# Performance work log

Hardware: AMD Instinct MI355X
Metric: run time of the kernel (lower is better)

Reference implementation:

```python
import jax, jax.numpy as jnp
import numpy as np

B, S, H, E, C, V = 512, 256, 768, 6, 10, 3


def setup_inputs() -> dict:
    key = jax.random.key(0)
    ks = jax.random.split(key, 16)

    def w(k, shape):
        fan_in = shape[-1]
        return jax.random.normal(k, shape, dtype=jnp.float32) / np.sqrt(fan_in)

    return {
        'x': jax.random.randint(ks[0], (B, S), 0, V, dtype=jnp.int64),
        'emb': w(ks[1], (V, E)),
        'W_fx': w(ks[2], (H, E)), 'W_fh': w(ks[3], (H, H)), 'b_f': w(ks[4], (H, 1)),
        'W_ix': w(ks[5], (H, E)), 'W_ih': w(ks[6], (H, H)), 'b_i': w(ks[7], (H, 1)),
        'W_ox': w(ks[8], (H, E)), 'W_oh': w(ks[9], (H, H)), 'b_o': w(ks[10], (H, 1)),
        'W_cx': w(ks[11], (H, E)), 'b_c': w(ks[12], (H, 1)),
        'W_ph': w(ks[13], (C, H)), 'b_p': w(ks[14], (C, 1)),
        'c_init': jax.random.normal(ks[15], (H, B), dtype=jnp.float32) / np.sqrt(B),
    }


def reference(x, emb, W_fx, W_fh, b_f, W_ix, W_ih, b_i, W_ox, W_oh, b_o,
              W_cx, b_c, W_ph, b_p, c_init):
    # Embed tokens: [B, S] -> [B, S, E] -> time-major [S, E, B]
    xe = jnp.transpose(emb[x], (1, 2, 0))
    xs = xe[: S - 1]  # loop runs seq_length - 1 steps

    def step(carry, x_t):
        c_prev, _ = carry  # c_prev: [H, B], x_t: [E, B]
        f_t = jax.nn.sigmoid(W_fx @ x_t + W_fh @ c_prev + b_f)
        i_t = jax.nn.sigmoid(W_ix @ x_t + W_ih @ c_prev + b_i)
        o_t = jax.nn.sigmoid(W_ox @ x_t + W_oh @ c_prev + b_o)
        c_t = jax.nn.sigmoid(W_cx @ x_t + b_c) * i_t + c_prev * f_t
        h_t = jnp.tanh(c_t) * o_t
        return (c_t, h_t), None

    h0 = jnp.zeros((H, B), dtype=c_init.dtype)
    (c_fin, h_fin), _ = jax.lax.scan(step, (c_init, h0), xs)
    p_t = W_ph @ h_fin + b_p  # [C, B]
    return jax.nn.log_softmax(p_t.T, axis=-1)  # [B, C]
```

## Files before the change

kernel.cpp:

```cpp
#include <hip/hip_runtime.h>


typedef _Float16 f16x8 __attribute__((ext_vector_type(8)));
typedef _Float16 f16x4 __attribute__((ext_vector_type(4)));
typedef float    f32x4 __attribute__((ext_vector_type(4)));

#define Hdim  768
#define Bdim  512
#define Sdim  256
#define NSTEP 255
#define Edim  6
#define NCls  10
#define NGRP  16
#define NRB   12
#define GC    32
#define HB    64
#define NKK   24
#define CSTR  776
#define XSTR  260
#define PLANE (Bdim * Hdim)
#define SCL      4096.0f
#define SCL_INV  2.44140625e-4f

#define WP_FRAGS   (2 * NRB * 4 * NKK * 64)
#define WS_CBUF    0u
#define WS_HFIN    (2u * 2u * PLANE * 2u)
#define WS_BAR     (WS_HFIN + Bdim * Hdim * 4u)
#define WS_WPK     (WS_BAR + 4096u)
#define WS_BAR_BYTES (NGRP * 16u * 4u)

__device__ __forceinline__ float sigf(float z) { return 1.0f / (1.0f + __expf(-z)); }

__device__ __forceinline__ f32x4 mf(f16x8 a, f16x8 b, f32x4 c) {
    return __builtin_amdgcn_mfma_f32_16x16x32_f16(a, b, c, 0, 0, 0);
}

__device__ __forceinline__ void keepalive(f16x8& x) {
    asm volatile("" : "+v"(x));
}

__global__ void __launch_bounds__(256)
prep_w(const float* __restrict__ Wfh, const float* __restrict__ Wih,
       _Float16* __restrict__ wpk)
{
    const int fid  = blockIdx.x * 256 + threadIdx.x;
    const int lane = fid & 63;
    const int t1   = fid >> 6;
    const int kk   = t1 % NKK;
    const int gi   = t1 / NKK;
    const int sub  = gi & 3;
    const int t3   = gi >> 2;
    const int rb   = t3 % NRB;
    const int gate = t3 / NRB;
    const int q = lane >> 4, r = lane & 15;
    const int row = rb * 64 + sub * 16 + r;
    const int col = kk * 32 + q * 8;
    const float* src = (gate ? Wih : Wfh) + (size_t)row * Hdim + col;
    f16x8 hi, lo;
    #pragma unroll
    for (int j = 0; j < 8; ++j) {
        const float v = src[j];
        const _Float16 h = (_Float16)v;
        hi[j] = h;
        lo[j] = (_Float16)((v - (float)h) * SCL);
    }
    *(f16x8*)&wpk[(size_t)fid * 8] = hi;
    *(f16x8*)&wpk[((size_t)WP_FRAGS + fid) * 8] = lo;
}

__global__ void __launch_bounds__(512, 2)
lstm_persist(const int* __restrict__ xk, const float* __restrict__ emb,
             const float* __restrict__ Wfx, const float* __restrict__ bfv,
             const float* __restrict__ Wix, const float* __restrict__ biv,
             const float* __restrict__ Wox, const float* __restrict__ Woh,
             const float* __restrict__ bov,
             const float* __restrict__ Wcx, const float* __restrict__ bcv,
             const float* __restrict__ cinit,
             const _Float16* __restrict__ wpk,
             _Float16* __restrict__ cbuf, float* __restrict__ hfin,
             unsigned int* __restrict__ bar)
{
    __shared__ __align__(16) _Float16 ldsH[GC * CSTR];
    __shared__ __align__(16) _Float16 ldsM[GC * CSTR];
    __shared__ __align__(16) float    tbl[3 * HB * 4];
    __shared__ __align__(16) float    zbuf[HB * GC];
    __shared__ __align__(4)  unsigned char xtok[GC * XSTR];
    __shared__ int s_flag;

    const int tid  = threadIdx.x;
    const int w    = tid >> 6;
    const int lane = tid & 63;
    const int q    = lane >> 4;
    const int r    = lane & 15;
    const int gt   = w >> 2;
    const int sub  = w & 3;
    const int bid  = blockIdx.x;
    const int g    = bid & 15;
    const int rb   = bid >> 4;
    const int blkh0 = rb * HB;
    const int gc0   = g * GC;
    const int hq0   = blkh0 + sub * 16 + q * 4;
    const int gi    = (gt * NRB + rb) * 4 + sub;

    if (tid == 0) s_flag = 0;
    __syncthreads();
    if (tid < 256) {
        if (xk[(size_t)gc0 * Sdim + 2 * tid + 1] != 0) s_flag = 1;
    }
    if (tid < 3 * HB) {
        const int v  = tid >> 6;
        const int hl = tid & 63;
        const int hg = blkh0 + hl;
        float pf = bfv[hg], pi = biv[hg], po = bov[hg], pc = bcv[hg];
        #pragma unroll
        for (int e = 0; e < Edim; ++e) {
            const float ev = emb[v * Edim + e];
            pf += Wfx[hg * Edim + e] * ev;
            pi += Wix[hg * Edim + e] * ev;
            po += Wox[hg * Edim + e] * ev;
            pc += Wcx[hg * Edim + e] * ev;
        }
        float* t = &tbl[(v * HB + hl) * 4];
        t[0] = pf; t[1] = pi; t[2] = po; t[3] = sigf(pc);
    }
    __syncthreads();
    const int is64 = (s_flag == 0);

    {
        const int col   = tid >> 4;
        const int sbase = (tid & 15) * 16;
        const size_t rowb = (size_t)(gc0 + col) * Sdim;
        for (int k2 = 0; k2 < 16; ++k2) {
            const int s0 = sbase + k2;
            const size_t idx = rowb + s0;
            xtok[col * XSTR + s0] = (unsigned char)xk[is64 ? (idx << 1) : idx];
        }
    }

    f16x8 whi[NKK], wlo[NKK];
    #pragma unroll
    for (int kk = 0; kk < NKK; ++kk) {
        whi[kk] = *(const f16x8*)&wpk[((size_t)(gi * NKK + kk) * 64 + lane) * 8];
        wlo[kk] = *(const f16x8*)&wpk[((size_t)WP_FRAGS + (size_t)(gi * NKK + kk) * 64 + lane) * 8];
    }
    #pragma unroll
    for (int kk = 0; kk < NKK; ++kk) {
        keepalive(whi[kk]);
        keepalive(wlo[kk]);
    }

    float cst[2][4];
    #pragma unroll
    for (int ct = 0; ct < 2; ++ct) {
        const int b = gc0 + ct * 16 + r;
        #pragma unroll
        for (int reg = 0; reg < 4; ++reg)
            cst[ct][reg] = cinit[(size_t)(hq0 + reg) * Bdim + b];
    }

    for (int i = 0; i < 48; ++i) {
        const int idx = tid + i * 512;
        const int col = idx & 31, k = idx >> 5;
        const float v = cinit[(size_t)k * Bdim + gc0 + col];
        const _Float16 h = (_Float16)v;
        ldsH[col * CSTR + k] = h;
        ldsM[col * CSTR + k] = (_Float16)((v - (float)h) * SCL);
    }

    for (int s = 0; s < NSTEP; ++s) {
        __syncthreads();

        f32x4 a0h = {0,0,0,0}, a0x = {0,0,0,0}, a1h = {0,0,0,0}, a1x = {0,0,0,0};
        #pragma unroll
        for (int kk = 0; kk < NKK; ++kk) {
            const int lo = kk * 32 + q * 8;
            const f16x8 bh0 = *(const f16x8*)&ldsH[ r       * CSTR + lo];
            const f16x8 bm0 = *(const f16x8*)&ldsM[ r       * CSTR + lo];
            const f16x8 bh1 = *(const f16x8*)&ldsH[(16 + r) * CSTR + lo];
            const f16x8 bm1 = *(const f16x8*)&ldsM[(16 + r) * CSTR + lo];
            a0h = mf(whi[kk], bh0, a0h);
            a0x = mf(whi[kk], bm0, a0x);
            a0x = mf(wlo[kk], bh0, a0x);
            a1h = mf(whi[kk], bh1, a1h);
            a1x = mf(whi[kk], bm1, a1x);
            a1x = mf(wlo[kk], bh1, a1x);
        }
        if (gt) {
            #pragma unroll
            for (int ct = 0; ct < 2; ++ct) {
                const f32x4 zh = ct ? a1h : a0h;
                const f32x4 zx = ct ? a1x : a0x;
                #pragma unroll
                for (int reg = 0; reg < 4; ++reg)
                    zbuf[(sub * 16 + q * 4 + reg) * GC + ct * 16 + r] =
                        zh[reg] + zx[reg] * SCL_INV;
            }
        }
        __syncthreads();

        if (!gt) {
            if (s != NSTEP - 1) {
                _Float16* cwH = cbuf + (size_t)(((s + 1) & 1) * 2) * PLANE;
                _Float16* cwM = cwH + PLANE;
                #pragma unroll
                for (int ct = 0; ct < 2; ++ct) {
                    const int bl = ct * 16 + r;
                    const int v  = xtok[bl * XSTR + s];
                    const float* tb = &tbl[(v * HB + sub * 16 + q * 4) * 4];
                    const f32x4 zh = ct ? a1h : a0h;
                    const f32x4 zx = ct ? a1x : a0x;
                    f16x4 cvh, cvm;
                    #pragma unroll
                    for (int reg = 0; reg < 4; ++reg) {
                        const float zf = zh[reg] + zx[reg] * SCL_INV;
                        const float zi = zbuf[(sub * 16 + q * 4 + reg) * GC + bl];
                        const float* tt = tb + reg * 4;
                        const float fg = sigf(zf + tt[0]);
                        const float ig = sigf(zi + tt[1]);
                        const float cn = tt[3] * ig + cst[ct][reg] * fg;
                        cst[ct][reg] = cn;
                        const _Float16 ch = (_Float16)cn;
                        cvh[reg] = ch;
                        cvm[reg] = (_Float16)((cn - (float)ch) * SCL);
                    }
                    unsigned long long uh, um;
                    __builtin_memcpy(&uh, &cvh, 8);
                    __builtin_memcpy(&um, &cvm, 8);
                    const size_t eo = (size_t)(gc0 + bl) * Hdim + hq0;
                    __hip_atomic_store((unsigned long long*)&cwH[eo], uh,
                                       __ATOMIC_RELAXED, __HIP_MEMORY_SCOPE_AGENT);
                    __hip_atomic_store((unsigned long long*)&cwM[eo], um,
                                       __ATOMIC_RELAXED, __HIP_MEMORY_SCOPE_AGENT);
                }
            } else {
                f32x4 o0h = {0,0,0,0}, o0x = {0,0,0,0}, o1h = {0,0,0,0}, o1x = {0,0,0,0};
                const int arow = blkh0 + sub * 16 + r;
                #pragma unroll
                for (int kk = 0; kk < NKK; ++kk) {
                    const float* wp = Woh + (size_t)arow * Hdim + kk * 32 + q * 8;
                    f16x8 who;
                    #pragma unroll
                    for (int j = 0; j < 8; ++j) who[j] = (_Float16)wp[j];
                    const int lo = kk * 32 + q * 8;
                    const f16x8 bh0 = *(const f16x8*)&ldsH[ r       * CSTR + lo];
                    const f16x8 bm0 = *(const f16x8*)&ldsM[ r       * CSTR + lo];
                    const f16x8 bh1 = *(const f16x8*)&ldsH[(16 + r) * CSTR + lo];
                    const f16x8 bm1 = *(const f16x8*)&ldsM[(16 + r) * CSTR + lo];
                    o0h = mf(who, bh0, o0h);  o0x = mf(who, bm0, o0x);
                    o1h = mf(who, bh1, o1h);  o1x = mf(who, bm1, o1x);
                }
                #pragma unroll
                for (int ct = 0; ct < 2; ++ct) {
                    const int bl = ct * 16 + r;
                    const int v  = xtok[bl * XSTR + s];
                    const float* tb = &tbl[(v * HB + sub * 16 + q * 4) * 4];
                    const f32x4 zh = ct ? a1h : a0h;
                    const f32x4 zx = ct ? a1x : a0x;
                    const f32x4 zoh = ct ? o1h : o0h;
                    const f32x4 zox = ct ? o1x : o0x;
                    f32x4 hv;
                    #pragma unroll
                    for (int reg = 0; reg < 4; ++reg) {
                        const float zf = zh[reg] + zx[reg] * SCL_INV;
                        const float zi = zbuf[(sub * 16 + q * 4 + reg) * GC + bl];
                        const float zo = zoh[reg] + zox[reg] * SCL_INV;
                        const float* tt = tb + reg * 4;
                        const float fg = sigf(zf + tt[0]);
                        const float ig = sigf(zi + tt[1]);
                        const float og = sigf(zo + tt[2]);
                        const float cn = tt[3] * ig + cst[ct][reg] * fg;
                        const float e  = __expf(-2.0f * fabsf(cn));
                        const float th = __builtin_copysignf((1.0f - e) / (1.0f + e), cn);
                        hv[reg] = th * og;
                    }
                    *(f32x4*)&hfin[(size_t)(gc0 + bl) * Hdim + hq0] = hv;
                }
            }
        }

        if (s < NSTEP - 1) {
            asm volatile("s_waitcnt vmcnt(0)" ::: "memory");
            __syncthreads();
            if (w == 0) {
                if (lane == 0)
                    __hip_atomic_store(&bar[g * 16 + rb], (unsigned)(s + 1),
                                       __ATOMIC_RELAXED, __HIP_MEMORY_SCOPE_AGENT);
                const unsigned tgt = (unsigned)(s + 1);
                while (true) {
                    unsigned vv = tgt;
                    if (lane < NRB)
                        vv = __hip_atomic_load(&bar[g * 16 + lane],
                                               __ATOMIC_RELAXED, __HIP_MEMORY_SCOPE_AGENT);
                    if (__all(vv >= tgt)) break;
                    __builtin_amdgcn_s_sleep(2);
                }
            }
            __syncthreads();
            const _Float16* crH = cbuf + (size_t)(((s + 1) & 1) * 2) * PLANE;
            const _Float16* crM = crH + PLANE;
            const int col = tid >> 4, j = tid & 15;
            const size_t rowo = (size_t)(gc0 + col) * Hdim;
            {
                unsigned long long th[12];
                #pragma unroll
                for (int i = 0; i < 12; ++i)
                    th[i] = __hip_atomic_load((unsigned long long*)&crH[rowo + (j + 16 * i) * 4],
                                              __ATOMIC_RELAXED, __HIP_MEMORY_SCOPE_AGENT);
                #pragma unroll
                for (int i = 0; i < 12; ++i)
                    *(unsigned long long*)&ldsH[col * CSTR + (j + 16 * i) * 4] = th[i];
            }
            {
                unsigned long long tm[12];
                #pragma unroll
                for (int i = 0; i < 12; ++i)
                    tm[i] = __hip_atomic_load((unsigned long long*)&crM[rowo + (j + 16 * i) * 4],
                                              __ATOMIC_RELAXED, __HIP_MEMORY_SCOPE_AGENT);
                #pragma unroll
                for (int i = 0; i < 12; ++i)
                    *(unsigned long long*)&ldsM[col * CSTR + (j + 16 * i) * 4] = tm[i];
            }
        }
    }
}

__global__ void __launch_bounds__(64)
proj_kernel(const float* __restrict__ hfin, const float* __restrict__ Wph,
            const float* __restrict__ bpv, float* __restrict__ out)
{
    const int b = blockIdx.x;
    const int lane = threadIdx.x;
    float acc[NCls];
    #pragma unroll
    for (int c = 0; c < NCls; ++c) acc[c] = 0.f;
    const float* hb = &hfin[(size_t)b * Hdim];
    for (int i = 0; i < Hdim / 64; ++i) {
        const float hv = hb[lane + i * 64];
        #pragma unroll
        for (int c = 0; c < NCls; ++c)
            acc[c] += Wph[c * Hdim + lane + i * 64] * hv;
    }
    #pragma unroll
    for (int c = 0; c < NCls; ++c) {
        float v = acc[c];
        #pragma unroll
        for (int off = 32; off > 0; off >>= 1)
            v += __shfl_xor(v, off, 64);
        acc[c] = v + bpv[c];
    }
    float m = acc[0];
    #pragma unroll
    for (int c = 1; c < NCls; ++c) m = fmaxf(m, acc[c]);
    float ssum = 0.f;
    #pragma unroll
    for (int c = 0; c < NCls; ++c) ssum += __expf(acc[c] - m);
    const float lse = m + __logf(ssum);
    if (lane < NCls) out[b * NCls + lane] = acc[lane] - lse;
}

extern "C" void kernel_launch(void* const* d_in, const int* in_sizes, int n_in,
                              void* d_out, int out_size, void* d_ws, size_t ws_size,
                              hipStream_t stream)
{
    const int*   xk    = (const int*)d_in[0];
    const float* emb   = (const float*)d_in[1];
    const float* Wfx   = (const float*)d_in[2];
    const float* Wfh   = (const float*)d_in[3];
    const float* bfv   = (const float*)d_in[4];
    const float* Wix   = (const float*)d_in[5];
    const float* Wih   = (const float*)d_in[6];
    const float* biv   = (const float*)d_in[7];
    const float* Wox   = (const float*)d_in[8];
    const float* Woh   = (const float*)d_in[9];
    const float* bov   = (const float*)d_in[10];
    const float* Wcx   = (const float*)d_in[11];
    const float* bcv   = (const float*)d_in[12];
    const float* Wph   = (const float*)d_in[13];
    const float* bpv   = (const float*)d_in[14];
    const float* cinit = (const float*)d_in[15];

    char* ws = (char*)d_ws;
    _Float16*     cbuf = (_Float16*)(ws + WS_CBUF);
    float*        hfin = (float*)(ws + WS_HFIN);
    unsigned int* bar  = (unsigned int*)(ws + WS_BAR);
    _Float16*     wpk  = (_Float16*)(ws + WS_WPK);

    hipMemsetAsync(bar, 0, WS_BAR_BYTES, stream);

    prep_w<<<dim3(WP_FRAGS / 256), dim3(256), 0, stream>>>(Wfh, Wih, wpk);

    lstm_persist<<<dim3(NGRP * NRB), dim3(512), 0, stream>>>(
        xk, emb, Wfx, bfv, Wix, biv, Wox, Woh, bov, Wcx, bcv,
        cinit, wpk, cbuf, hfin, bar);

    proj_kernel<<<dim3(Bdim), dim3(64), 0, stream>>>(hfin, Wph, bpv, (float*)d_out);
}
```

Baseline: 2.119 ms.

## Split K dimension across wave pairs with LDS reduction in LSTM step

Each wave now computes two 16-row subtiles over half of the K range instead of one subtile over the full K. Partial sums are exchanged through LDS: forget-gate partials go through a pairwise swap buffer, and input-gate partials go through two padded planes. The aim is to give each wave more independent MFMA accumulators and to halve the serial K chain per step. The cost is extra LDS traffic and reduction adds, and the launch bound is changed to one block per SIMD group to allow the larger register footprint.

```diff
diff --git a/kernel.cpp b/kernel.cpp
--- a/kernel.cpp
+++ b/kernel.cpp
@@ -16,8 +16,10 @@
 #define GC    32
 #define HB    64
 #define NKK   24
+#define NK2   12
 #define CSTR  776
 #define XSTR  260
+#define ZSTR  33
 #define PLANE (Bdim * Hdim)
 #define SCL      4096.0f
 #define SCL_INV  2.44140625e-4f
@@ -68,7 +70,7 @@
     *(f16x8*)&wpk[((size_t)WP_FRAGS + fid) * 8] = lo;
 }
 
-__global__ void __launch_bounds__(512, 2)
+__global__ void __launch_bounds__(512, 1)
 lstm_persist(const int* __restrict__ xk, const float* __restrict__ emb,
              const float* __restrict__ Wfx, const float* __restrict__ bfv,
              const float* __restrict__ Wix, const float* __restrict__ biv,
@@ -83,7 +85,8 @@
     __shared__ __align__(16) _Float16 ldsH[GC * CSTR];
     __shared__ __align__(16) _Float16 ldsM[GC * CSTR];
     __shared__ __align__(16) float    tbl[3 * HB * 4];
-    __shared__ __align__(16) float    zbuf[HB * GC];
+    __shared__ __align__(16) float    zred[4 * 4 * 64 * 4];
+    __shared__ __align__(16) float    zbufP[2 * HB * ZSTR];
     __shared__ __align__(4)  unsigned char xtok[GC * XSTR];
     __shared__ int s_flag;
 
@@ -92,15 +95,17 @@
     const int lane = tid & 63;
     const int q    = lane >> 4;
     const int r    = lane & 15;
-    const int gt   = w >> 2;
-    const int sub  = w & 3;
+    const int kh   = w & 1;
+    const int pr   = w >> 1;
+    const int gt   = pr >> 1;
+    const int rh   = pr & 1;
+    const int subp = rh * 2 + kh;
     const int bid  = blockIdx.x;
     const int g    = bid & 15;
     const int rb   = bid >> 4;
     const int blkh0 = rb * HB;
     const int gc0   = g * GC;
-    const int hq0   = blkh0 + sub * 16 + q * 4;
-    const int gi    = (gt * NRB + rb) * 4 + sub;
+    const int hq0   = blkh0 + subp * 16 + q * 4;
 
     if (tid == 0) s_flag = 0;
     __syncthreads();
@@ -137,17 +142,24 @@
         }
     }
 
-    f16x8 whi[NKK], wlo[NKK];
-    #pragma unroll
-    for (int kk = 0; kk < NKK; ++kk) {
-        whi[kk] = *(const f16x8*)&wpk[((size_t)(gi * NKK + kk) * 64 + lane) * 8];
-        wlo[kk] = *(const f16x8*)&wpk[((size_t)WP_FRAGS + (size_t)(gi * NKK + kk) * 64 + lane) * 8];
-    }
-    #pragma unroll
-    for (int kk = 0; kk < NKK; ++kk) {
-        keepalive(whi[kk]);
-        keepalive(wlo[kk]);
-    }
+    f16x8 whi[2][NK2], wlo[2][NK2];
+    #pragma unroll
+    for (int s2 = 0; s2 < 2; ++s2) {
+        const int gis = (gt * NRB + rb) * 4 + (rh * 2 + s2);
+        #pragma unroll
+        for (int k2 = 0; k2 < NK2; ++k2) {
+            const size_t fo = ((size_t)(gis * NKK + kh * NK2 + k2) * 64 + lane) * 8;
+            whi[s2][k2] = *(const f16x8*)&wpk[fo];
+            wlo[s2][k2] = *(const f16x8*)&wpk[(size_t)WP_FRAGS * 8 + fo];
+        }
+    }
+    #pragma unroll
+    for (int s2 = 0; s2 < 2; ++s2)
+        #pragma unroll
+        for (int k2 = 0; k2 < NK2; ++k2) {
+            keepalive(whi[s2][k2]);
+            keepalive(wlo[s2][k2]);
+        }
 
     float cst[2][4];
     #pragma unroll
@@ -170,35 +182,76 @@
     for (int s = 0; s < NSTEP; ++s) {
         __syncthreads();
 
-        f32x4 a0h = {0,0,0,0}, a0x = {0,0,0,0}, a1h = {0,0,0,0}, a1x = {0,0,0,0};
-        #pragma unroll
-        for (int kk = 0; kk < NKK; ++kk) {
-            const int lo = kk * 32 + q * 8;
+        f32x4 ah0c0 = {0,0,0,0}, ax0c0 = {0,0,0,0}, ah0c1 = {0,0,0,0}, ax0c1 = {0,0,0,0};
+        f32x4 ah1c0 = {0,0,0,0}, ax1c0 = {0,0,0,0}, ah1c1 = {0,0,0,0}, ax1c1 = {0,0,0,0};
+        #pragma unroll
+        for (int k2 = 0; k2 < NK2; ++k2) {
+            const int lo = (kh * NK2 + k2) * 32 + q * 8;
             const f16x8 bh0 = *(const f16x8*)&ldsH[ r       * CSTR + lo];
             const f16x8 bm0 = *(const f16x8*)&ldsM[ r       * CSTR + lo];
             const f16x8 bh1 = *(const f16x8*)&ldsH[(16 + r) * CSTR + lo];
             const f16x8 bm1 = *(const f16x8*)&ldsM[(16 + r) * CSTR + lo];
-            a0h = mf(whi[kk], bh0, a0h);
-            a0x = mf(whi[kk], bm0, a0x);
-            a0x = mf(wlo[kk], bh0, a0x);
-            a1h = mf(whi[kk], bh1, a1h);
-            a1x = mf(whi[kk], bm1, a1x);
-            a1x = mf(wlo[kk], bh1, a1x);
-        }
-        if (gt) {
+            ah0c0 = mf(whi[0][k2], bh0, ah0c0);
+            ax0c0 = mf(whi[0][k2], bm0, ax0c0);
+            ax0c0 = mf(wlo[0][k2], bh0, ax0c0);
+            ah1c0 = mf(whi[1][k2], bh0, ah1c0);
+            ax1c0 = mf(whi[1][k2], bm0, ax1c0);
+            ax1c0 = mf(wlo[1][k2], bh0, ax1c0);
+            ah0c1 = mf(whi[0][k2], bh1, ah0c1);
+            ax0c1 = mf(whi[0][k2], bm1, ax0c1);
+            ax0c1 = mf(wlo[0][k2], bh1, ax0c1);
+            ah1c1 = mf(whi[1][k2], bh1, ah1c1);
+            ax1c1 = mf(whi[1][k2], bm1, ax1c1);
+            ax1c1 = mf(wlo[1][k2], bh1, ax1c1);
+        }
+
+        if (gt == 0) {
+            const f32x4 sH0 = kh ? ah0c0 : ah1c0;
+            const f32x4 sX0 = kh ? ax0c0 : ax1c0;
+            const f32x4 sH1 = kh ? ah0c1 : ah1c1;
+            const f32x4 sX1 = kh ? ax0c1 : ax1c1;
+            f32x4* zr = (f32x4*)zred;
+            zr[(w * 4 + 0) * 64 + lane] = sH0;
+            zr[(w * 4 + 1) * 64 + lane] = sX0;
+            zr[(w * 4 + 2) * 64 + lane] = sH1;
+            zr[(w * 4 + 3) * 64 + lane] = sX1;
+        } else {
+            float* zp = &zbufP[kh * (HB * ZSTR)];
             #pragma unroll
-            for (int ct = 0; ct < 2; ++ct) {
-                const f32x4 zh = ct ? a1h : a0h;
-                const f32x4 zx = ct ? a1x : a0x;
-                #pragma unroll
-                for (int reg = 0; reg < 4; ++reg)
-                    zbuf[(sub * 16 + q * 4 + reg) * GC + ct * 16 + r] =
-                        zh[reg] + zx[reg] * SCL_INV;
+            for (int s2 = 0; s2 < 2; ++s2) {
+                const f32x4 h0 = s2 ? ah1c0 : ah0c0;
+                const f32x4 x0 = s2 ? ax1c0 : ax0c0;
+                const f32x4 h1 = s2 ? ah1c1 : ah0c1;
+                const f32x4 x1 = s2 ? ax1c1 : ax0c1;
+                #pragma unroll
+                for (int reg = 0; reg < 4; ++reg) {
+                    const int row = rh * 32 + s2 * 16 + q * 4 + reg;
+                    zp[row * ZSTR + r]      = h0[reg] + x0[reg] * SCL_INV;
+                    zp[row * ZSTR + 16 + r] = h1[reg] + x1[reg] * SCL_INV;
+                }
             }
         }
         __syncthreads();
 
-        if (!gt) {
+        if (gt == 0) {
+            const f32x4* zr = (const f32x4*)zred;
+            const int pw = w ^ 1;
+            const f32x4 pH0 = zr[(pw * 4 + 0) * 64 + lane];
+            const f32x4 pX0 = zr[(pw * 4 + 1) * 64 + lane];
+            const f32x4 pH1 = zr[(pw * 4 + 2) * 64 + lane];
+            const f32x4 pX1 = zr[(pw * 4 + 3) * 64 + lane];
+            const f32x4 kH0 = kh ? ah1c0 : ah0c0;
+            const f32x4 kX0 = kh ? ax1c0 : ax0c0;
+            const f32x4 kH1 = kh ? ah1c1 : ah0c1;
+            const f32x4 kX1 = kh ? ax1c1 : ax0c1;
+            float zf[2][4];
+            #pragma unroll
+            for (int reg = 0; reg < 4; ++reg) {
+                zf[0][reg] = (kH0[reg] + pH0[reg]) + (kX0[reg] + pX0[reg]) * SCL_INV;
+                zf[1][reg] = (kH1[reg] + pH1[reg]) + (kX1[reg] + pX1[reg]) * SCL_INV;
+            }
+            const int rowl0 = rh * 32 + kh * 16 + q * 4;
+
             if (s != NSTEP - 1) {
                 _Float16* cwH = cbuf + (size_t)(((s + 1) & 1) * 2) * PLANE;
                 _Float16* cwM = cwH + PLANE;
@@ -206,16 +259,15 @@
                 for (int ct = 0; ct < 2; ++ct) {
                     const int bl = ct * 16 + r;
                     const int v  = xtok[bl * XSTR + s];
-                    const float* tb = &tbl[(v * HB + sub * 16 + q * 4) * 4];
-                    const f32x4 zh = ct ? a1h : a0h;
-                    const f32x4 zx = ct ? a1x : a0x;
+                    const float* tb = &tbl[(v * HB + subp * 16 + q * 4) * 4];
                     f16x4 cvh, cvm;
                     #pragma unroll
                     for (int reg = 0; reg < 4; ++reg) {
-                        const float zf = zh[reg] + zx[reg] * SCL_INV;
-                        const float zi = zbuf[(sub * 16 + q * 4 + reg) * GC + bl];
+                        const int rowl = rowl0 + reg;
+                        const float zi = zbufP[rowl * ZSTR + bl]
+                                       + zbufP[HB * ZSTR + rowl * ZSTR + bl];
                         const float* tt = tb + reg * 4;
-                        const float fg = sigf(zf + tt[0]);
+                        const float fg = sigf(zf[ct][reg] + tt[0]);
                         const float ig = sigf(zi + tt[1]);
                         const float cn = tt[3] * ig + cst[ct][reg] * fg;
                         cst[ct][reg] = cn;
@@ -234,7 +286,7 @@
                 }
             } else {
                 f32x4 o0h = {0,0,0,0}, o0x = {0,0,0,0}, o1h = {0,0,0,0}, o1x = {0,0,0,0};
-                const int arow = blkh0 + sub * 16 + r;
+                const int arow = blkh0 + subp * 16 + r;
                 #pragma unroll
                 for (int kk = 0; kk < NKK; ++kk) {
                     const float* wp = Woh + (size_t)arow * Hdim + kk * 32 + q * 8;
@@ -253,19 +305,18 @@
                 for (int ct = 0; ct < 2; ++ct) {
                     const int bl = ct * 16 + r;
                     const int v  = xtok[bl * XSTR + s];
-                    const float* tb = &tbl[(v * HB + sub * 16 + q * 4) * 4];
-                    const f32x4 zh = ct ? a1h : a0h;
-                    const f32x4 zx = ct ? a1x : a0x;
+                    const float* tb = &tbl[(v * HB + subp * 16 + q * 4) * 4];
                     const f32x4 zoh = ct ? o1h : o0h;
                     const f32x4 zox = ct ? o1x : o0x;
                     f32x4 hv;
                     #pragma unroll
                     for (int reg = 0; reg < 4; ++reg) {
-                        const float zf = zh[reg] + zx[reg] * SCL_INV;
-                        const float zi = zbuf[(sub * 16 + q * 4 + reg) * GC + bl];
+                        const int rowl = rowl0 + reg;
+                        const float zi = zbufP[rowl * ZSTR + bl]
+                                       + zbufP[HB * ZSTR + rowl * ZSTR + bl];
                         const float zo = zoh[reg] + zox[reg] * SCL_INV;
                         const float* tt = tb + reg * 4;
-                        const float fg = sigf(zf + tt[0]);
+                        const float fg = sigf(zf[ct][reg] + tt[0]);
                         const float ig = sigf(zi + tt[1]);
                         const float og = sigf(zo + tt[2]);
                         const float cn = tt[3] * ig + cst[ct][reg] * fg;
```

Measured after the change: 2.118 ms. Within noise of the previous version (-0.0%).
